# Performance work log

Hardware: AMD Instinct MI355X
Metric: run time of the kernel (lower is better)

The kernel has to match this reference:

```python
import jax, jax.numpy as jnp
import numpy as np
jax.config.update("jax_enable_x64", True)

K = 10            # num_digits
NUM_CLASSES = 10  # digit classes 0..9
EQ_TOKEN = 28
PRIMES = np.array([7, 11, 13, 17, 19, 23, 29, 31, 37], dtype=np.int64)
TWO_PI = 2.0 * np.pi
M_TOTAL = int(np.prod(PRIMES.astype(object)))  # product of primes ~2.47e11 (needs int64)
_crt = []
for p in PRIMES:
    Mi = M_TOTAL // int(p)
    _crt.append((Mi * pow(Mi, -1, int(p))) % M_TOTAL)
CRT_C = jnp.array(_crt, dtype=jnp.int64)                 # [P] CRT mixing coefficients
POW10 = jnp.array([[pow(10, k, int(p)) for k in range(K)] for p in PRIMES], dtype=jnp.float32)  # [P,K]
PR_F = jnp.array(PRIMES, dtype=jnp.float32)
PR_I = jnp.array(PRIMES, dtype=jnp.int64)
POW10_DEC = jnp.array([10 ** k for k in range(K)], dtype=jnp.int64)
_op = np.full(64, -1, dtype=np.int64)
_op[20:25] = np.arange(5)  # tokens 20..24 -> ops add,sub,mul,exp,div
OP_TABLE = jnp.array(_op)


def encode(d):
    # d [B,S,K] soft base-10 digits -> RNS circle encoding [B,S,P,2]
    theta = TWO_PI * jnp.einsum('bsk,pk->bsp', d, POW10) / PR_F
    return jnp.stack([jnp.cos(theta), jnp.sin(theta)], axis=-1)


def decode_residues(circle):
    # [B,S,P,2] -> integer residues mod p, [B,S,P] int64
    theta = jnp.arctan2(circle[..., 1], circle[..., 0])
    r = jnp.round(theta / TWO_PI * PR_F).astype(jnp.int64)
    return jnp.mod(r, PR_I)


def circle_add(a, b):
    ca, sa = a[..., 0], a[..., 1]
    cb, sb = b[..., 0], b[..., 1]
    return jnp.stack([ca * cb - sa * sb, sa * cb + ca * sb], axis=-1)


def circle_sub(a, b):
    ca, sa = a[..., 0], a[..., 1]
    cb, sb = b[..., 0], b[..., 1]
    return jnp.stack([ca * cb + sa * sb, sa * cb - ca * sb], axis=-1)


def modpow(base, exp, mod):
    # elementwise modular exponentiation, exponents < 64 (6 square-and-multiply steps)
    res = jnp.ones_like(base)
    b = jnp.mod(base, mod)
    e = exp
    for _ in range(6):
        res = jnp.where((e & 1) == 1, (res * b) % mod, res)
        b = (b * b) % mod
        e = e >> 1
    return res


def crt(residues):
    # CRT reconstruction: [B,S,P] -> [B,S] int64 in [0, M_TOTAL)
    return jnp.mod(jnp.sum(residues * CRT_C, axis=-1), M_TOTAL)


def crt_signed(residues):
    n = crt(residues)
    return jnp.where(n > M_TOTAL // 2, n - M_TOTAL, n)


def int_to_digits(n):
    # [B,S] int64 -> [B,S,K] float base-10 digits, LSB-first
    return ((n[..., None] // POW10_DEC) % 10).astype(jnp.float32)


def int_to_digits_signed(n):
    sign = (n < 0).astype(jnp.float32)[..., None]
    return jnp.concatenate([int_to_digits(jnp.abs(n)), sign], axis=-1)  # [B,S,K+1]


def decode_all_ops(a_c, b_c):
    # All 5 operations decoded to digit vectors -> [B,S,5K+1]
    ra = decode_residues(a_c)
    rb = decode_residues(b_c)
    add_d = int_to_digits(crt(decode_residues(circle_add(a_c, b_c))))
    sub_d = int_to_digits_signed(crt_signed(decode_residues(circle_sub(a_c, b_c))))
    mul_d = int_to_digits(crt((ra * rb) % PR_I))
    exp_d = int_to_digits(crt(modpow(ra, rb, PR_I)))
    inv = modpow(rb, PR_I - 2, PR_I)  # Fermat inverse
    div_r = jnp.where(rb == 0, 0, (ra * inv) % PR_I)
    div_d = int_to_digits(crt(div_r))
    return jnp.concatenate([add_d, sub_d, mul_d, exp_d, div_d], axis=-1)


def select_op(results, input_ids):
    # [B,S,5K+1] -> [B,S,K+1]: pick the relevant operation per sequence
    B, S, _ = results.shape
    pad = jnp.zeros((B, S, 1), results.dtype)
    ops = jnp.stack([
        jnp.concatenate([results[..., 0:K], pad], -1),
        results[..., K:2 * K + 1],
        jnp.concatenate([results[..., 2 * K + 1:3 * K + 1], pad], -1),
        jnp.concatenate([results[..., 3 * K + 1:4 * K + 1], pad], -1),
        jnp.concatenate([results[..., 4 * K + 1:5 * K + 1], pad], -1),
    ], axis=-2)  # [B,S,5,K+1]
    is_op = OP_TABLE[jnp.clip(input_ids, 0, 63)] >= 0
    op_pos = jnp.argmax(is_op, axis=1)  # first operator position per sequence
    op_tok = jnp.take_along_axis(input_ids, op_pos[:, None], axis=1)[:, 0]
    op_idx = OP_TABLE[jnp.clip(op_tok, 0, 63)]
    gidx = jnp.broadcast_to(jnp.clip(op_idx, 0, 4)[:, None, None, None], (B, S, 1, K + 1))
    sel = jnp.take_along_axis(ops, gidx, axis=-2)[..., 0, :]
    valid = (op_idx >= 0).astype(results.dtype)[:, None, None]
    return sel * valid


def reorder_msb(res):
    # LSB-first digits -> MSB-first, -1 sentinel past the last significant digit
    digits = res[..., :K]
    sign = res[..., K:]
    idx = jnp.arange(K)
    nz = digits != 0
    highest = jnp.max(jnp.where(nz, idx, -1), axis=-1)
    num_sig = jnp.where(jnp.any(nz, axis=-1), highest + 1, 1)
    src = jnp.clip(num_sig[..., None] - 1 - idx, 0, K - 1)
    msb = jnp.take_along_axis(digits, src, axis=-1)
    msb = jnp.where(idx < num_sig[..., None], msb, -1.0)
    return jnp.concatenate([msb, sign], axis=-1)


def setup_inputs() -> dict:
    key = jax.random.key(0)
    ks = jax.random.split(key, 6)
    B, S, D, MH = 16, 2048, 768, 128
    h = jax.random.normal(ks[0], (B, S, D), dtype=jnp.float32)
    input_ids = jax.random.randint(ks[1], (B, S), 0, 50, dtype=jnp.int64)
    W1 = jax.random.normal(ks[2], (D, MH), dtype=jnp.float32) * 0.02
    b1 = jnp.zeros((MH,), jnp.float32)
    W2 = jax.random.normal(ks[3], (MH, 2 * K * NUM_CLASSES), dtype=jnp.float32) * 0.02
    b2 = jnp.zeros((2 * K * NUM_CLASSES,), jnp.float32)
    Winj = jax.random.normal(ks[4], (K + 1, D), dtype=jnp.float32) * 0.001  # injector_init_std
    binj = jnp.zeros((D,), jnp.float32)
    gate_logit = jnp.array(-2.0, jnp.float32)  # gate_init_logit
    return {"h": h, "W1": W1, "b1": b1, "W2": W2, "b2": b2,
            "Winj": Winj, "binj": binj, "gate_logit": gate_logit, "input_ids": input_ids}


def reference(h, W1, b1, W2, b2, Winj, binj, gate_logit, input_ids):
    B, S, D = h.shape
    # OperandExtractor: per-token MLP -> soft digits for operands a and b
    hid = jax.nn.relu(h @ W1 + b1)
    logits = (hid @ W2 + b2).reshape(B, S, 2, K, NUM_CLASSES)
    probs = jax.nn.softmax(logits, axis=-1)
    dig = jnp.einsum('bsokc,c->bsok', probs, jnp.arange(NUM_CLASSES, dtype=h.dtype))
    d_a, d_b = dig[..., 0, :], dig[..., 1, :]
    # RNSCircleEncoder (frozen)
    a_c = encode(d_a)
    b_c = encode(d_b)
    # ArithmeticCompute + CRT decode: detached (torch.no_grad in original)
    results = jax.lax.stop_gradient(decode_all_ops(a_c, b_c).astype(h.dtype))
    sel = select_op(results, input_ids)
    msb = reorder_msb(sel)
    # ResultInjector: gated linear injection into the residual stream
    inj = msb @ Winj + binj
    h_prime = h + jax.nn.sigmoid(gate_logit) * inj
    # only inject for sequences containing the '=' token
    has_eq = jnp.any(input_ids == EQ_TOKEN, axis=1).astype(h.dtype)[:, None, None]
    h_prime = h + (h_prime - h) * has_eq
    return h_prime, d_a, d_b
```

## Files before the change

kernel.cpp:

```cpp
#include <hip/hip_runtime.h>

typedef unsigned short u16;
typedef unsigned int   u32;
typedef unsigned long long u64;

typedef __attribute__((ext_vector_type(8))) short short8;
typedef __attribute__((ext_vector_type(4))) float f32x4;

#define DEV static __device__ __forceinline__

__constant__ float POW10F[9][10] = {
  {1,3,2,6,4,5,1,3,2,6},
  {1,10,1,10,1,10,1,10,1,10},
  {1,10,9,12,3,4,1,10,9,12},
  {1,10,15,14,4,6,9,5,16,7},
  {1,10,5,12,6,3,11,15,17,18},
  {1,10,8,11,18,19,6,14,2,20},
  {1,10,13,14,24,8,22,17,25,18},
  {1,10,7,8,18,25,2,20,14,16},
  {1,10,26,1,10,26,1,10,26,1},
};

#define M_TOTAL  247357937827ull
#define M_HALF   123678968913ull

DEV u16 f2bf_rne(float f){
  u32 u = __float_as_uint(f);
  return (u16)((u + 0x7FFFu + ((u >> 16) & 1u)) >> 16);
}
DEV float bf2f(u16 v){ return __uint_as_float(((u32)v) << 16); }

DEV short8 pack_bf16(float4 a, float4 b){
  union { short8 s; u32 u[4]; } r;
  r.u[0] = (__float_as_uint(a.x) >> 16) | (__float_as_uint(a.y) & 0xFFFF0000u);
  r.u[1] = (__float_as_uint(a.z) >> 16) | (__float_as_uint(a.w) & 0xFFFF0000u);
  r.u[2] = (__float_as_uint(b.x) >> 16) | (__float_as_uint(b.y) & 0xFFFF0000u);
  r.u[3] = (__float_as_uint(b.z) >> 16) | (__float_as_uint(b.w) & 0xFFFF0000u);
  return r.s;
}

DEV void load_lds16(const void* g, void* l){
  __builtin_amdgcn_global_load_lds((const __attribute__((address_space(1))) void*)g,
                                   (__attribute__((address_space(3))) void*)l, 16, 0, 0);
}

DEV int modpow6(int b, int e, int p){
  int res = 1; b %= p;
  #pragma unroll
  for (int i = 0; i < 6; ++i){
    if (e & 1) res = (res * b) % p;
    b = (b * b) % p;
    e >>= 1;
  }
  return res;
}

__global__ void prelude_kernel(const int* __restrict__ ids, const float* __restrict__ W1,
                               const float* __restrict__ W2, int* __restrict__ op_idx,
                               float* __restrict__ has_eq, u16* __restrict__ w1f,
                               u16* __restrict__ w2f){
  __shared__ int smin[256];
  __shared__ int seq[256];
  int bid = blockIdx.x, tid = threadIdx.x;
  if (bid < 16){
    int b = bid;
    int best = 2048, eq = 0;
    for (int i = tid; i < 2048; i += 256){
      int t = ids[b * 2048 + i];
      if (t >= 20 && t < 25) best = min(best, i);
      eq |= (t == 28) ? 1 : 0;
    }
    smin[tid] = best; seq[tid] = eq;
    __syncthreads();
    for (int s = 128; s > 0; s >>= 1){
      if (tid < s){ smin[tid] = min(smin[tid], smin[tid + s]); seq[tid] |= seq[tid + s]; }
      __syncthreads();
    }
    if (tid == 0){
      int op = -1;
      if (smin[0] < 2048) op = ids[b * 2048 + smin[0]] - 20;
      op_idx[b] = op;
      has_eq[b] = seq[0] ? 1.0f : 0.0f;
    }
  } else {
    int t = (bid - 16) * 256 + tid;
    if (t < 12288){
      int blk = t >> 6, L = t & 63;
      int T = blk >> 3, b = blk & 7;
      int q = L >> 4, ln = L & 15;
      #pragma unroll
      for (int j = 0; j < 8; ++j){
        int k = 32 * T + 8 * q + j;
        int n = 16 * b + ln;
        w1f[(size_t)blk * 512 + L * 8 + j] = f2bf_rne(W1[k * 128 + n]);
      }
    } else {
      int t2 = t - 12288;
      int blk = t2 >> 6, L = t2 & 63;
      int ts = blk / 13, b2 = blk % 13;
      int q = L >> 4, ln = L & 15;
      #pragma unroll
      for (int j = 0; j < 8; ++j){
        int k = 32 * ts + 8 * q + j;
        int n = 16 * b2 + ln;
        w2f[(size_t)blk * 512 + L * 8 + j] = (n < 200) ? f2bf_rne(W2[k * 200 + n]) : (u16)0;
      }
    }
  }
}

__launch_bounds__(256, 2)
__global__ void mega_kernel(const float* __restrict__ h, const u16* __restrict__ w1f,
                            const u16* __restrict__ w2f, const float* __restrict__ b1,
                            const float* __restrict__ b2, const float* __restrict__ Winj,
                            const float* __restrict__ binj, const float* __restrict__ gate,
                            const int* __restrict__ op_idx_ws, const float* __restrict__ has_eq_ws,
                            float* __restrict__ dout){
  __shared__ __align__(16) char lds[49152];
  u16*   wbuf     = (u16*)lds;
  char*  tail     = lds + 32768;
  float* digits_s = (float*)tail;
  float* tab_s    = (float*)(tail + 5120);
  u64*   ops_s    = (u64*)(tail + 9728);
  float* msbv     = (float*)(tail + 12288);
  u16*   hidf     = (u16*)tail;
  float* winj_s   = (float*)lds;
  float* binj_s   = (float*)(lds + 33792);

  const int tid  = threadIdx.x;
  const int w    = tid >> 6;
  const int lane = tid & 63;
  const int ln   = lane & 15, q = lane >> 4;
  const int wg   = blockIdx.x;
  const int tok0 = wg * 64;
  const int gtok = tok0 + w * 16 + ln;
  const int batch = wg >> 5;

  const int   op = op_idx_ws[batch];
  const float G  = has_eq_ws[batch] * (1.0f / (1.0f + __expf(-gate[0])));

  float b1v[8];
  #pragma unroll
  for (int b = 0; b < 8; ++b) b1v[b] = b1[ln + 16 * b];
  float b2v[13];
  #pragma unroll
  for (int b = 0; b < 13; ++b){ int n = ln + 16 * b; b2v[b] = (n < 200) ? b2[n] : 0.0f; }

  f32x4 acc[8];
  #pragma unroll
  for (int b = 0; b < 8; ++b) acc[b] = (f32x4)0.0f;

  const float4* ap = (const float4*)(h + (size_t)gtok * 768);
  float4 xa[2], xb[2];
  #pragma unroll
  for (int i = 0; i < 4; ++i){
    int bl = w * 4 + i;
    load_lds16(w1f + (size_t)(((bl >> 3)) * 8 + (bl & 7)) * 512 + lane * 8,
               wbuf + bl * 512);
  }
  #pragma unroll
  for (int t = 0; t < 2; ++t){ xa[t] = ap[t * 8 + q * 2]; xb[t] = ap[t * 8 + q * 2 + 1]; }

  #pragma unroll
  for (int c = 0; c < 12; ++c){
    __syncthreads();
    const u16* cur = wbuf + (c & 1) * 8192;
    if (c < 11){
      u16* nxt = wbuf + ((c + 1) & 1) * 8192;
      #pragma unroll
      for (int i = 0; i < 4; ++i){
        int bl = w * 4 + i;
        int T  = (c + 1) * 2 + (bl >> 3);
        load_lds16(w1f + (size_t)(T * 8 + (bl & 7)) * 512 + lane * 8, nxt + bl * 512);
      }
    }
    short8 af[2];
    #pragma unroll
    for (int t = 0; t < 2; ++t) af[t] = pack_bf16(xa[t], xb[t]);
    if (c < 11){
      const float4* ap2 = ap + (c + 1) * 16;
      #pragma unroll
      for (int t = 0; t < 2; ++t){ xa[t] = ap2[t * 8 + q * 2]; xb[t] = ap2[t * 8 + q * 2 + 1]; }
    }
    #pragma unroll
    for (int t = 0; t < 2; ++t){
      #pragma unroll
      for (int b = 0; b < 8; ++b){
        short8 bf = *(const short8*)(cur + (t * 8 + b) * 512 + lane * 8);
        acc[b] = __builtin_amdgcn_mfma_f32_16x16x32_bf16(af[t], bf, acc[b], 0, 0, 0);
      }
    }
  }

  #pragma unroll
  for (int b = 0; b < 8; ++b){
    int t2 = b >> 1;
    int q2 = ((b & 1) << 1) | (ln >> 3);
    int j  = ln & 7;
    #pragma unroll
    for (int r = 0; r < 4; ++r){
      float v = fmaxf(acc[b][r] + b1v[b], 0.0f);
      int L2 = (q2 << 4) | (q * 4 + r);
      hidf[w * 2048 + t2 * 512 + L2 * 8 + j] = (u16)(__float_as_uint(v) >> 16);
    }
  }
  __syncthreads();

  short8 a2[4];
  #pragma unroll
  for (int t = 0; t < 4; ++t) a2[t] = *(const short8*)(hidf + w * 2048 + t * 512 + lane * 8);
  f32x4 acc2[13];
  #pragma unroll
  for (int b = 0; b < 13; ++b) acc2[b] = (f32x4)0.0f;
  #pragma unroll
  for (int b = 0; b < 13; ++b){
    #pragma unroll
    for (int t = 0; t < 4; ++t){
      short8 bf = *(const short8*)(w2f + (size_t)(t * 13 + b) * 512 + lane * 8);
      acc2[b] = __builtin_amdgcn_mfma_f32_16x16x32_bf16(a2[t], bf, acc2[b], 0, 0, 0);
    }
  }

  #pragma unroll
  for (int b = 0; b < 13; ++b){
    #pragma unroll
    for (int r = 0; r < 4; ++r){
      float v = acc2[b][r] + b2v[b];
      wbuf[w * 4096 + (q * 4 + r) * 212 + ln + 16 * b] = (u16)(__float_as_uint(v) >> 16);
    }
  }
  __syncthreads();

  #pragma unroll
  for (int i = 0; i < 5; ++i){
    int task = tid + i * 256;
    int tok = task / 20, slot = task % 20;
    const u16* lp = wbuf + (tok >> 4) * 4096 + (tok & 15) * 212 + slot * 10;
    float v[10];
    #pragma unroll
    for (int k = 0; k < 10; ++k) v[k] = bf2f(lp[k]);
    float mx = v[0];
    #pragma unroll
    for (int k = 1; k < 10; ++k) mx = fmaxf(mx, v[k]);
    float s = 0.0f, sd = 0.0f;
    #pragma unroll
    for (int k = 0; k < 10; ++k){
      float e = __expf(v[k] - mx);
      s += e; sd += e * (float)k;
    }
    float dig = sd / s;
    digits_s[tok * 20 + slot] = dig;
    int gt = tok0 + tok;
    int o = slot / 10, k10 = slot % 10;
    dout[(size_t)25165824 + (size_t)o * 327680 + (size_t)gt * 10 + k10] = dig;
  }
  __syncthreads();

  #pragma unroll
  for (int i = 0; i < 8; ++i){
    int idx = tid + i * 256;
    float4 vsrc = *(const float4*)(Winj + (size_t)idx * 4);
    *(float4*)(winj_s + (size_t)idx * 4) = vsrc;
  }

  #pragma unroll
  for (int i = 0; i < 5; ++i){
    int task = tid + i * 256;
    if (task < 1152){
      int tok = task / 18, rm = task % 18;
      int ab = rm / 9, pi = rm % 9;
      float t = 0.0f;
      #pragma unroll
      for (int k = 0; k < 10; ++k) t += digits_s[tok * 20 + ab * 10 + k] * POW10F[pi][k];
      tab_s[tok * 18 + ab * 9 + pi] = t;
    }
  }
  __syncthreads();

  {
    int idx = 2048 + (tid >> 1) + ((tid & 1) ? 224 : 0);
  }
  if (tid < 224){
    #pragma unroll
    for (int i = 0; i < 2; ++i){
      int idx = 2048 + tid + i * 224;
      if (idx < 2496){
        const float* src = (idx < 2112) ? (Winj + (size_t)idx * 4)
                                        : (binj + (size_t)(idx - 2112) * 4);
        float4 vsrc = *(const float4*)src;
        *(float4*)(winj_s + (size_t)idx * 4) = vsrc;
      }
    }
  }

  {
    constexpr int PR[9] = {7, 11, 13, 17, 19, 23, 29, 31, 37};
    constexpr u64 CRTC[9] = {
      35336848261ull, 224870852570ull, 114165202074ull, 218257003965ull,
      78113032998ull, 53773464745ull, 68236672504ull, 223420072876ull, 220616539143ull
    };
    #pragma unroll
    for (int rep = 0; rep < 2; ++rep){
      int task = tid + rep * 256;
      if (task < 320){
        int o5 = task >> 6, tok = task & 63;
        u64 acc64 = 0;
        #pragma unroll
        for (int pi = 0; pi < 9; ++pi){
          const int p = PR[pi];
          float ta = tab_s[tok * 18 + pi], tb = tab_s[tok * 18 + 9 + pi];
          int r;
          if (o5 == 0){
            r = __float2int_rn(ta + tb) % p;
          } else if (o5 == 1){
            int s = __float2int_rn(ta - tb) % p;
            r = (s < 0) ? s + p : s;
          } else {
            int ra = __float2int_rn(ta) % p;
            int rb = __float2int_rn(tb) % p;
            if (o5 == 2) r = (ra * rb) % p;
            else if (o5 == 3) r = modpow6(ra, rb, p);
            else r = (rb == 0) ? 0 : (ra * modpow6(rb, p - 2, p)) % p;
          }
          acc64 += (u64)r * CRTC[pi];
        }
        u64 n = acc64 % M_TOTAL;
        int sign = 0;
        u64 un = n;
        if (o5 == 1 && n > M_HALF){ sign = 1; un = M_TOTAL - n; }
        u64 pk = 0;
        #pragma unroll
        for (int k = 0; k < 10; ++k){ pk |= (un % 10ull) << (4 * k); un /= 10ull; }
        pk |= ((u64)sign) << 40;
        ops_s[tok * 5 + o5] = pk;
      }
    }
  }
  __syncthreads();

  if (tid < 64){
    int tok = tid;
    u64 pk = (op >= 0) ? ops_s[tok * 5 + op] : 0ull;
    int g[10]; int hi = -1;
    #pragma unroll
    for (int k = 0; k < 10; ++k){
      g[k] = (int)((pk >> (4 * k)) & 15ull);
      if (g[k] != 0) hi = k;
    }
    int ns = (hi >= 0) ? hi + 1 : 1;
    #pragma unroll
    for (int i = 0; i < 10; ++i)
      msbv[tok * 12 + i] = (i < ns) ? (float)g[ns - 1 - i] : -1.0f;
    msbv[tok * 12 + 10] = (float)((pk >> 40) & 1ull);
    msbv[tok * 12 + 11] = 0.0f;
  }
  __syncthreads();

  if (tid < 192){
    float4 wv[11];
    #pragma unroll
    for (int j = 0; j < 11; ++j) wv[j] = *(const float4*)(winj_s + j * 768 + tid * 4);
    float4 bj = *(const float4*)(binj_s + tid * 4);
    const size_t base = (size_t)tok0 * 768 + tid * 4;
    #pragma unroll 4
    for (int tt = 0; tt < 64; ++tt){
      float4 m0 = *(const float4*)(msbv + tt * 12);
      float4 m1 = *(const float4*)(msbv + tt * 12 + 4);
      float4 m2 = *(const float4*)(msbv + tt * 12 + 8);
      float4 hv = *(const float4*)(h + base + (size_t)tt * 768);
      float ix = bj.x, iy = bj.y, iz = bj.z, iw = bj.w;
      ix += m0.x*wv[0].x + m0.y*wv[1].x + m0.z*wv[2].x + m0.w*wv[3].x
          + m1.x*wv[4].x + m1.y*wv[5].x + m1.z*wv[6].x + m1.w*wv[7].x
          + m2.x*wv[8].x + m2.y*wv[9].x + m2.z*wv[10].x;
      iy += m0.x*wv[0].y + m0.y*wv[1].y + m0.z*wv[2].y + m0.w*wv[3].y
          + m1.x*wv[4].y + m1.y*wv[5].y + m1.z*wv[6].y + m1.w*wv[7].y
          + m2.x*wv[8].y + m2.y*wv[9].y + m2.z*wv[10].y;
      iz += m0.x*wv[0].z + m0.y*wv[1].z + m0.z*wv[2].z + m0.w*wv[3].z
          + m1.x*wv[4].z + m1.y*wv[5].z + m1.z*wv[6].z + m1.w*wv[7].z
          + m2.x*wv[8].z + m2.y*wv[9].z + m2.z*wv[10].z;
      iw += m0.x*wv[0].w + m0.y*wv[1].w + m0.z*wv[2].w + m0.w*wv[3].w
          + m1.x*wv[4].w + m1.y*wv[5].w + m1.z*wv[6].w + m1.w*wv[7].w
          + m2.x*wv[8].w + m2.y*wv[9].w + m2.z*wv[10].w;
      float4 o;
      o.x = hv.x + G * ix; o.y = hv.y + G * iy;
      o.z = hv.z + G * iz; o.w = hv.w + G * iw;
      *(float4*)(dout + base + (size_t)tt * 768) = o;
    }
  }
}

extern "C" void kernel_launch(void* const* d_in, const int* in_sizes, int n_in,
                              void* d_out, int out_size, void* d_ws, size_t ws_size,
                              hipStream_t stream){
  const float* h    = (const float*)d_in[0];
  const float* W1   = (const float*)d_in[1];
  const float* b1   = (const float*)d_in[2];
  const float* W2   = (const float*)d_in[3];
  const float* b2   = (const float*)d_in[4];
  const float* Winj = (const float*)d_in[5];
  const float* binj = (const float*)d_in[6];
  const float* gate = (const float*)d_in[7];
  const int*   ids  = (const int*)d_in[8];
  float* dout = (float*)d_out;

  char* ws = (char*)d_ws;
  int*   op_idx = (int*)(ws + 0);
  float* has_eq = (float*)(ws + 64);
  u16*   w1f    = (u16*)(ws + 256);
  u16*   w2f    = (u16*)(ws + 256 + 196608);

  prelude_kernel<<<77, 256, 0, stream>>>(ids, W1, W2, op_idx, has_eq, w1f, w2f);
  mega_kernel<<<512, 256, 0, stream>>>(h, w1f, w2f, b1, b2, Winj, binj, gate,
                                       op_idx, has_eq, dout);
}
```

Measured before the change: 234.2 us.

## Load W1 fragments straight into registers and drop LDS staging of Winj

The first GEMM no longer stages W1 tiles through LDS with async global-to-LDS copies and a block barrier per chunk. Each wave now loads its B fragments directly from global memory into double-buffered registers over 24 K-steps, and the per-wave hidden-tile barrier is removed. The Winj/binj copy into LDS is also removed; the injection step reads them directly from global. This removes barriers and LDS round trips, but every wave now fetches the full W1 on its own, which is four times the global/L2 traffic per block, and it uses more registers.

```diff
diff --git a/kernel.cpp b/kernel.cpp
--- a/kernel.cpp
+++ b/kernel.cpp
@@ -37,11 +37,6 @@
   r.u[2] = (__float_as_uint(b.x) >> 16) | (__float_as_uint(b.y) & 0xFFFF0000u);
   r.u[3] = (__float_as_uint(b.z) >> 16) | (__float_as_uint(b.w) & 0xFFFF0000u);
   return r.s;
-}
-
-DEV void load_lds16(const void* g, void* l){
-  __builtin_amdgcn_global_load_lds((const __attribute__((address_space(1))) void*)g,
-                                   (__attribute__((address_space(3))) void*)l, 16, 0, 0);
 }
 
 DEV int modpow6(int b, int e, int p){
@@ -117,15 +112,13 @@
                             const int* __restrict__ op_idx_ws, const float* __restrict__ has_eq_ws,
                             float* __restrict__ dout){
   __shared__ __align__(16) char lds[49152];
-  u16*   wbuf     = (u16*)lds;
+  u16*   lbuf     = (u16*)lds;
   char*  tail     = lds + 32768;
   float* digits_s = (float*)tail;
   float* tab_s    = (float*)(tail + 5120);
   u64*   ops_s    = (u64*)(tail + 9728);
   float* msbv     = (float*)(tail + 12288);
   u16*   hidf     = (u16*)tail;
-  float* winj_s   = (float*)lds;
-  float* binj_s   = (float*)(lds + 33792);
 
   const int tid  = threadIdx.x;
   const int w    = tid >> 6;
@@ -150,46 +143,32 @@
   #pragma unroll
   for (int b = 0; b < 8; ++b) acc[b] = (f32x4)0.0f;
 
-  const float4* ap = (const float4*)(h + (size_t)gtok * 768);
-  float4 xa[2], xb[2];
-  #pragma unroll
-  for (int i = 0; i < 4; ++i){
-    int bl = w * 4 + i;
-    load_lds16(w1f + (size_t)(((bl >> 3)) * 8 + (bl & 7)) * 512 + lane * 8,
-               wbuf + bl * 512);
-  }
-  #pragma unroll
-  for (int t = 0; t < 2; ++t){ xa[t] = ap[t * 8 + q * 2]; xb[t] = ap[t * 8 + q * 2 + 1]; }
-
-  #pragma unroll
-  for (int c = 0; c < 12; ++c){
-    __syncthreads();
-    const u16* cur = wbuf + (c & 1) * 8192;
-    if (c < 11){
-      u16* nxt = wbuf + ((c + 1) & 1) * 8192;
+  const float* hrow = h + (size_t)gtok * 768;
+  float4 ha[2], hb[2];
+  short8 bfr[2][8];
+
+  ha[0] = *(const float4*)(hrow + 8 * q);
+  hb[0] = *(const float4*)(hrow + 8 * q + 4);
+  #pragma unroll
+  for (int b = 0; b < 8; ++b)
+    bfr[0][b] = *(const short8*)(w1f + (size_t)b * 512 + lane * 8);
+
+  #pragma unroll 2
+  for (int c = 0; c < 24; ++c){
+    const int s = c & 1, ns = s ^ 1;
+    if (c < 23){
+      const float* hp = hrow + (c + 1) * 32 + 8 * q;
+      ha[ns] = *(const float4*)hp;
+      hb[ns] = *(const float4*)(hp + 4);
+      const u16* wp = w1f + (size_t)(c + 1) * 4096 + lane * 8;
       #pragma unroll
-      for (int i = 0; i < 4; ++i){
-        int bl = w * 4 + i;
-        int T  = (c + 1) * 2 + (bl >> 3);
-        load_lds16(w1f + (size_t)(T * 8 + (bl & 7)) * 512 + lane * 8, nxt + bl * 512);
-      }
-    }
-    short8 af[2];
-    #pragma unroll
-    for (int t = 0; t < 2; ++t) af[t] = pack_bf16(xa[t], xb[t]);
-    if (c < 11){
-      const float4* ap2 = ap + (c + 1) * 16;
-      #pragma unroll
-      for (int t = 0; t < 2; ++t){ xa[t] = ap2[t * 8 + q * 2]; xb[t] = ap2[t * 8 + q * 2 + 1]; }
-    }
-    #pragma unroll
-    for (int t = 0; t < 2; ++t){
-      #pragma unroll
-      for (int b = 0; b < 8; ++b){
-        short8 bf = *(const short8*)(cur + (t * 8 + b) * 512 + lane * 8);
-        acc[b] = __builtin_amdgcn_mfma_f32_16x16x32_bf16(af[t], bf, acc[b], 0, 0, 0);
-      }
-    }
+      for (int b = 0; b < 8; ++b)
+        bfr[ns][b] = *(const short8*)(wp + (size_t)b * 512);
+    }
+    short8 af = pack_bf16(ha[s], hb[s]);
+    #pragma unroll
+    for (int b = 0; b < 8; ++b)
+      acc[b] = __builtin_amdgcn_mfma_f32_16x16x32_bf16(af, bfr[s][b], acc[b], 0, 0, 0);
   }
 
   #pragma unroll
@@ -204,7 +183,6 @@
       hidf[w * 2048 + t2 * 512 + L2 * 8 + j] = (u16)(__float_as_uint(v) >> 16);
     }
   }
-  __syncthreads();
 
   short8 a2[4];
   #pragma unroll
@@ -226,7 +204,7 @@
     #pragma unroll
     for (int r = 0; r < 4; ++r){
       float v = acc2[b][r] + b2v[b];
-      wbuf[w * 4096 + (q * 4 + r) * 212 + ln + 16 * b] = (u16)(__float_as_uint(v) >> 16);
+      lbuf[w * 4096 + (q * 4 + r) * 212 + ln + 16 * b] = (u16)(__float_as_uint(v) >> 16);
     }
   }
   __syncthreads();
@@ -235,7 +213,7 @@
   for (int i = 0; i < 5; ++i){
     int task = tid + i * 256;
     int tok = task / 20, slot = task % 20;
-    const u16* lp = wbuf + (tok >> 4) * 4096 + (tok & 15) * 212 + slot * 10;
+    const u16* lp = lbuf + (tok >> 4) * 4096 + (tok & 15) * 212 + slot * 10;
     float v[10];
     #pragma unroll
     for (int k = 0; k < 10; ++k) v[k] = bf2f(lp[k]);
@@ -255,13 +233,6 @@
     dout[(size_t)25165824 + (size_t)o * 327680 + (size_t)gt * 10 + k10] = dig;
   }
   __syncthreads();
-
-  #pragma unroll
-  for (int i = 0; i < 8; ++i){
-    int idx = tid + i * 256;
-    float4 vsrc = *(const float4*)(Winj + (size_t)idx * 4);
-    *(float4*)(winj_s + (size_t)idx * 4) = vsrc;
-  }
 
   #pragma unroll
   for (int i = 0; i < 5; ++i){
@@ -276,22 +247,6 @@
     }
   }
   __syncthreads();
-
-  {
-    int idx = 2048 + (tid >> 1) + ((tid & 1) ? 224 : 0);
-  }
-  if (tid < 224){
-    #pragma unroll
-    for (int i = 0; i < 2; ++i){
-      int idx = 2048 + tid + i * 224;
-      if (idx < 2496){
-        const float* src = (idx < 2112) ? (Winj + (size_t)idx * 4)
-                                        : (binj + (size_t)(idx - 2112) * 4);
-        float4 vsrc = *(const float4*)src;
-        *(float4*)(winj_s + (size_t)idx * 4) = vsrc;
-      }
-    }
-  }
 
   {
     constexpr int PR[9] = {7, 11, 13, 17, 19, 23, 29, 31, 37};
@@ -359,8 +314,8 @@
   if (tid < 192){
     float4 wv[11];
     #pragma unroll
-    for (int j = 0; j < 11; ++j) wv[j] = *(const float4*)(winj_s + j * 768 + tid * 4);
-    float4 bj = *(const float4*)(binj_s + tid * 4);
+    for (int j = 0; j < 11; ++j) wv[j] = *(const float4*)(Winj + (size_t)j * 768 + tid * 4);
+    float4 bj = *(const float4*)(binj + tid * 4);
     const size_t base = (size_t)tok0 * 768 + tid * 4;
     #pragma unroll 4
     for (int tt = 0; tt < 64; ++tt){
```

Result: slower. 438.1 us (+87.0%).
